# Kernel tuning notes

Hardware: AMD Instinct MI355X
Metric: run time of the kernel (lower is better)

The kernel has to match this reference:

```python
import jax, jax.numpy as jnp
import numpy as np

D = 1024
K = 3  # depthwise conv kernel size, causal (left pad K-1)


def setup_inputs() -> dict:
    key = jax.random.key(0)
    ks = jax.random.split(key, 6)
    B, L = 16, 2048
    x = jax.random.normal(ks[0], (B, L, D), dtype=jnp.float32)
    s_in = 1.0 / np.sqrt(D)
    Win = jax.random.uniform(ks[1], (3 * D, D), minval=-s_in, maxval=s_in, dtype=jnp.float32)
    bin_ = jax.random.uniform(ks[2], (3 * D,), minval=-s_in, maxval=s_in, dtype=jnp.float32)
    # depthwise Conv1d weight (D, 1, K) -> stored as (D, K)
    s_c = 1.0 / np.sqrt(K)  # fan_in = in_channels/groups * K = K
    wconv = jax.random.uniform(ks[3], (D, K), minval=-s_c, maxval=s_c, dtype=jnp.float32)
    Wout = jax.random.uniform(ks[4], (D, D), minval=-s_in, maxval=s_in, dtype=jnp.float32)
    bout = jax.random.uniform(ks[5], (D,), minval=-s_in, maxval=s_in, dtype=jnp.float32)
    return {"x": x, "Win": Win, "bin_": bin_, "wconv": wconv, "Wout": Wout, "bout": bout}


def reference(x, Win, bin_, wconv, Wout, bout):
    # x: (B, L, D). in_proj -> (B, L, 3D); chunk along channel dim == last dim here
    BCx = jnp.einsum('bld,ed->ble', x, Win) + bin_
    Bg, Cg, xg = jnp.split(BCx, 3, axis=-1)  # each (B, L, D)
    Bx = Bg * xg
    L = Bx.shape[1]
    # causal depthwise conv: pad K-1 zeros on the left of time axis
    xp = jnp.pad(Bx, ((0, 0), (K - 1, 0), (0, 0)))
    conv_out = (wconv[:, 0] * xp[:, 0:L]
                + wconv[:, 1] * xp[:, 1:L + 1]
                + wconv[:, 2] * xp[:, 2:L + 2])  # (B, L, D)
    y = Cg * conv_out
    return jnp.einsum('bld,ed->ble', y, Wout) + bout
```

## Files before the change

kernel.cpp:

```cpp
#include <hip/hip_runtime.h>
#include <hip/hip_bf16.h>

#define D_    1024
#define LSEQ  2048
#define M_    32768
#define K_    1024
#define NT    16

typedef __bf16 bf16x8 __attribute__((ext_vector_type(8)));
typedef float  f32x4  __attribute__((ext_vector_type(4)));

__device__ __forceinline__ unsigned short f2bf(float f) {
  unsigned u = __float_as_uint(f);
  u += 0x7FFFu + ((u >> 16) & 1u);
  return (unsigned short)(u >> 16);
}
__device__ __forceinline__ float bf2f(unsigned short h) {
  return __uint_as_float(((unsigned)h) << 16);
}

__device__ __forceinline__ void gload_lds16(const void* g, void* l) {
  __builtin_amdgcn_global_load_lds((const __attribute__((address_space(1))) void*)g,
                                   (__attribute__((address_space(3))) void*)l,
                                   16, 0, 0);
}

#define FENCE() asm volatile("" ::: "memory")
#define RBAR()  do { FENCE(); __builtin_amdgcn_s_barrier(); FENCE(); } while (0)

#define NX4  (M_ * K_ / 4)
#define NW4  (3072 * K_ / 4)
#define NO4  (D_ * K_ / 4)
__global__ __launch_bounds__(256) void cvt_all(const float* __restrict__ x,
                                               const float* __restrict__ Win,
                                               const float* __restrict__ Wout,
                                               unsigned short* __restrict__ x_b,
                                               unsigned short* __restrict__ Win_b,
                                               unsigned short* __restrict__ Wout_b) {
  int i = blockIdx.x * 256 + threadIdx.x;
  const float* src;
  unsigned short* dst;
  int off;
  if (i < NX4)            { src = x;    dst = x_b;    off = i; }
  else if (i < NX4 + NW4) { src = Win;  dst = Win_b;  off = i - NX4; }
  else                    { src = Wout; dst = Wout_b; off = i - NX4 - NW4; }
  float4 v = ((const float4*)src)[off];
  ushort4 o;
  o.x = f2bf(v.x); o.y = f2bf(v.y); o.z = f2bf(v.z); o.w = f2bf(v.w);
  ((ushort4*)dst)[off] = o;
}


__device__ __forceinline__ void gemm_core256(char* smem,
    const unsigned short* aBase,
    const unsigned short* b0p, const unsigned short* b1p,
    const unsigned short* b2p, const unsigned short* b3p,
    f32x4 acc[8][4]) {
  const int tid  = threadIdx.x;
  const int lane = tid & 63;
  const int wm   = (tid >> 6) >> 2;
  const int wn   = (tid >> 6) & 3;
  const int quad = lane >> 4;
  const int l16  = lane & 15;
  const int swz  = (quad ^ (l16 & 7)) << 4;
  const int aRow = ((wm << 7) + l16) * 128 + swz;
  const int bRow = ((wn << 6) + l16) * 128 + swz;

  auto STAGE = [&](int t) {
    char* lb = smem + ((t & 1) << 16);
    const int k0 = t << 6;
#pragma unroll
    for (int i = 0; i < 4; ++i)
      gload_lds16(aBase + ((long)i << 16) + k0, lb + tid * 16 + i * 8192);
    gload_lds16(b0p + k0, lb + 32768 + tid * 16);
    gload_lds16(b1p + k0, lb + 32768 + tid * 16 + 8192);
    gload_lds16(b2p + k0, lb + 32768 + tid * 16 + 16384);
    gload_lds16(b3p + k0, lb + 32768 + tid * 16 + 24576);
  };

  STAGE(0);
  STAGE(1);
  asm volatile("s_waitcnt vmcnt(8)" ::: "memory");
  RBAR();

  bf16x8 av[4][2], b0[2][2], b1[2][2];

  for (int t = 0; t < NT; ++t) {
    const char* As = smem + ((t & 1) << 16);
    const char* Bs = As + 32768;

#pragma unroll
    for (int f = 0; f < 2; ++f) {
      const int o = bRow + f * 2048;
      b0[f][0] = *(const bf16x8*)(Bs + o);
      b0[f][1] = *(const bf16x8*)(Bs + (o ^ 64));
    }
#pragma unroll
    for (int f = 0; f < 4; ++f) {
      const int o = aRow + f * 2048;
      av[f][0] = *(const bf16x8*)(As + o);
      av[f][1] = *(const bf16x8*)(As + (o ^ 64));
    }
#pragma unroll
    for (int f = 0; f < 2; ++f) {
      const int o = bRow + (2 + f) * 2048;
      b1[f][0] = *(const bf16x8*)(Bs + o);
      b1[f][1] = *(const bf16x8*)(Bs + (o ^ 64));
    }
    RBAR();

    __builtin_amdgcn_s_setprio(1);
#pragma unroll
    for (int f = 0; f < 4; ++f)
#pragma unroll
      for (int gg = 0; gg < 2; ++gg) {
        f32x4 c = acc[f][gg];
        c = __builtin_amdgcn_mfma_f32_16x16x32_bf16(av[f][0], b0[gg][0], c, 0, 0, 0);
        c = __builtin_amdgcn_mfma_f32_16x16x32_bf16(av[f][1], b0[gg][1], c, 0, 0, 0);
        acc[f][gg] = c;
      }
    __builtin_amdgcn_s_setprio(0);
    RBAR();

    __builtin_amdgcn_s_setprio(1);
#pragma unroll
    for (int f = 0; f < 4; ++f) {
#pragma unroll
      for (int gg = 0; gg < 2; ++gg) {
        f32x4 c = acc[f][2 + gg];
        c = __builtin_amdgcn_mfma_f32_16x16x32_bf16(av[f][0], b1[gg][0], c, 0, 0, 0);
        c = __builtin_amdgcn_mfma_f32_16x16x32_bf16(av[f][1], b1[gg][1], c, 0, 0, 0);
        acc[f][2 + gg] = c;
      }
      const int o = aRow + (4 + f) * 2048;
      av[f][0] = *(const bf16x8*)(As + o);
      av[f][1] = *(const bf16x8*)(As + (o ^ 64));
    }
    __builtin_amdgcn_s_setprio(0);
    RBAR();

    __builtin_amdgcn_s_setprio(1);
#pragma unroll
    for (int f = 0; f < 4; ++f)
#pragma unroll
      for (int gg = 0; gg < 2; ++gg) {
        f32x4 c = acc[4 + f][2 + gg];
        c = __builtin_amdgcn_mfma_f32_16x16x32_bf16(av[f][0], b1[gg][0], c, 0, 0, 0);
        c = __builtin_amdgcn_mfma_f32_16x16x32_bf16(av[f][1], b1[gg][1], c, 0, 0, 0);
        acc[4 + f][2 + gg] = c;
      }
    __builtin_amdgcn_s_setprio(0);
    RBAR();

    if (t + 2 < NT) STAGE(t + 2);
    __builtin_amdgcn_s_setprio(1);
#pragma unroll
    for (int f = 0; f < 4; ++f)
#pragma unroll
      for (int gg = 0; gg < 2; ++gg) {
        f32x4 c = acc[4 + f][gg];
        c = __builtin_amdgcn_mfma_f32_16x16x32_bf16(av[f][0], b0[gg][0], c, 0, 0, 0);
        c = __builtin_amdgcn_mfma_f32_16x16x32_bf16(av[f][1], b0[gg][1], c, 0, 0, 0);
        acc[4 + f][gg] = c;
      }
    __builtin_amdgcn_s_setprio(0);

    if (t + 2 < NT) {
      asm volatile("s_waitcnt vmcnt(8)" ::: "memory");
      RBAR();
    } else if (t + 2 == NT) {
      asm volatile("s_waitcnt vmcnt(0)" ::: "memory");
      RBAR();
    }
  }
}

__global__ __launch_bounds__(512, 2) void gemm_inproj(const unsigned short* __restrict__ A,
                                                      const unsigned short* __restrict__ Wb,
                                                      const float* __restrict__ bin,
                                                      unsigned short* __restrict__ Bx,
                                                      unsigned short* __restrict__ Cg) {
  __shared__ __align__(16) char smem[131072];

  const int g  = blockIdx.x;
  const int u  = g >> 3;
  const int m0 = ((g & 7) + 8 * (u / 12)) * 256;
  const int c  = u % 12;
  const bool paired = (c < 8);

  const int tid  = threadIdx.x;
  const int lane = tid & 63;
  const int srow = ((tid >> 6) << 3) + (lane >> 3);
  const int sch  = (lane & 7) ^ (lane >> 3);

  const unsigned short* aBase = A + (long)(m0 + srow) * K_ + sch * 8;
  const unsigned short *b0p, *b1p, *b2p, *b3p;
  int n0;
  if (paired) {
    n0  = c * 128;
    b0p = Wb + (long)(n0 + srow) * K_ + sch * 8;
    b1p = b0p + (long)64 * K_;
    b2p = Wb + (long)(2048 + n0 + srow) * K_ + sch * 8;
    b3p = b2p + (long)64 * K_;
  } else {
    n0  = (c - 8) * 256;
    b0p = Wb + (long)(1024 + n0 + srow) * K_ + sch * 8;
    b1p = b0p + (long)64 * K_;
    b2p = b0p + (long)128 * K_;
    b3p = b0p + (long)192 * K_;
  }

  f32x4 acc[8][4] = {};
  gemm_core256(smem, aBase, b0p, b1p, b2p, b3p, acc);

  const int wm = (tid >> 6) >> 2, wn = (tid >> 6) & 3;
  const int quad = lane >> 4, l16 = lane & 15;
  float* tr = (float*)smem;

  float bvv[4];
#pragma unroll
  for (int ni = 0; ni < 4; ++ni) {
    int col = wn * 64 + ni * 16 + l16;
    bvv[ni] = paired ? ((col < 128) ? bin[n0 + col] : bin[2048 + n0 + col - 128])
                     : bin[1024 + n0 + col];
  }

  const int trr   = tid >> 4;
  const int tcc   = tid & 15;
  const int growb = m0 + ((trr >> 4) << 7) + (trr & 15);

#pragma unroll
  for (int mi = 0; mi < 8; ++mi) {
    __syncthreads();
#pragma unroll
    for (int ni = 0; ni < 4; ++ni) {
      int col = wn * 64 + ni * 16 + l16;
      f32x4 v = acc[mi][ni];
#pragma unroll
      for (int r = 0; r < 4; ++r)
        tr[(wm * 16 + quad * 4 + r) * 260 + col] = v[r] + bvv[ni];
    }
    __syncthreads();

    const int grow = growb + mi * 16;
    if (paired) {
#pragma unroll
      for (int j = 0; j < 2; ++j) {
        int cc = tcc * 4 + j * 64;
        f32x4 bg = *(const f32x4*)&tr[trr * 260 + cc];
        f32x4 xg = *(const f32x4*)&tr[trr * 260 + 128 + cc];
        ushort4 o;
        o.x = f2bf(bg[0] * xg[0]); o.y = f2bf(bg[1] * xg[1]);
        o.z = f2bf(bg[2] * xg[2]); o.w = f2bf(bg[3] * xg[3]);
        *(ushort4*)&Bx[(long)grow * D_ + n0 + cc] = o;
      }
    } else {
#pragma unroll
      for (int j = 0; j < 4; ++j) {
        int cc = tcc * 4 + j * 64;
        f32x4 v = *(const f32x4*)&tr[trr * 260 + cc];
        ushort4 o;
        o.x = f2bf(v[0]); o.y = f2bf(v[1]); o.z = f2bf(v[2]); o.w = f2bf(v[3]);
        *(ushort4*)&Cg[(long)grow * D_ + n0 + cc] = o;
      }
    }
  }
}

__global__ __launch_bounds__(256) void conv_mul(const unsigned short* __restrict__ Bx,
                                                const unsigned short* __restrict__ Cg,
                                                const float* __restrict__ wconv,
                                                unsigned short* __restrict__ y) {
  __shared__ float wt[3][D_];
  for (int i = threadIdx.x; i < D_; i += 256) {
    wt[0][i] = wconv[i * 3 + 0];
    wt[1][i] = wconv[i * 3 + 1];
    wt[2][i] = wconv[i * 3 + 2];
  }
  __syncthreads();

  int idx = blockIdx.x * 256 + threadIdx.x;
  int bl  = idx >> 7;
  int d8  = (idx & 127) * 8;
  int l   = bl & (LSEQ - 1);

  typedef unsigned short us8 __attribute__((ext_vector_type(8)));
  us8 zz = {0, 0, 0, 0, 0, 0, 0, 0};
  us8 x0 = *(const us8*)&Bx[(long)bl * D_ + d8];
  us8 x1 = (l >= 1) ? *(const us8*)&Bx[(long)(bl - 1) * D_ + d8] : zz;
  us8 x2 = (l >= 2) ? *(const us8*)&Bx[(long)(bl - 2) * D_ + d8] : zz;
  us8 cg = *(const us8*)&Cg[(long)bl * D_ + d8];

  us8 o;
#pragma unroll
  for (int j = 0; j < 8; ++j) {
    float conv = wt[0][d8 + j] * bf2f(x2[j]) + wt[1][d8 + j] * bf2f(x1[j])
               + wt[2][d8 + j] * bf2f(x0[j]);
    o[j] = f2bf(bf2f(cg[j]) * conv);
  }
  *(us8*)&y[(long)bl * D_ + d8] = o;
}

__global__ __launch_bounds__(512, 2) void gemm_out(const unsigned short* __restrict__ A,
                                                   const unsigned short* __restrict__ Wb,
                                                   const float* __restrict__ bias,
                                                   float* __restrict__ Out) {
  __shared__ __align__(16) char smem[131072];

  const int g  = blockIdx.x;
  const int u  = g >> 3;
  const int m0 = ((g & 7) + 8 * (u >> 2)) * 256;
  const int n0 = (u & 3) * 256;

  const int tid  = threadIdx.x;
  const int lane = tid & 63;
  const int srow = ((tid >> 6) << 3) + (lane >> 3);
  const int sch  = (lane & 7) ^ (lane >> 3);

  const unsigned short* aBase = A + (long)(m0 + srow) * K_ + sch * 8;
  const unsigned short* b0p   = Wb + (long)(n0 + srow) * K_ + sch * 8;

  f32x4 acc[8][4] = {};
  gemm_core256(smem, aBase, b0p, b0p + (long)64 * K_, b0p + (long)128 * K_,
               b0p + (long)192 * K_, acc);

  const int wm = (tid >> 6) >> 2, wn = (tid >> 6) & 3;
  const int quad = lane >> 4, l16 = lane & 15;
  float* tr = (float*)smem;

  float bvv[4];
#pragma unroll
  for (int ni = 0; ni < 4; ++ni)
    bvv[ni] = bias[n0 + wn * 64 + ni * 16 + l16];

  const int trr   = tid >> 4;
  const int tcc   = tid & 15;
  const int growb = m0 + ((trr >> 4) << 7) + (trr & 15);

#pragma unroll
  for (int mi = 0; mi < 8; ++mi) {
    __syncthreads();
#pragma unroll
    for (int ni = 0; ni < 4; ++ni) {
      int col = wn * 64 + ni * 16 + l16;
      f32x4 v = acc[mi][ni];
#pragma unroll
      for (int r = 0; r < 4; ++r)
        tr[(wm * 16 + quad * 4 + r) * 260 + col] = v[r] + bvv[ni];
    }
    __syncthreads();

    const int grow = growb + mi * 16;
#pragma unroll
    for (int j = 0; j < 4; ++j) {
      int cc = tcc * 4 + j * 64;
      *(f32x4*)&Out[(long)grow * D_ + n0 + cc] = *(const f32x4*)&tr[trr * 260 + cc];
    }
  }
}

extern "C" void kernel_launch(void* const* d_in, const int* in_sizes, int n_in,
                              void* d_out, int out_size, void* d_ws, size_t ws_size,
                              hipStream_t stream) {
  const float* x     = (const float*)d_in[0];
  const float* Win   = (const float*)d_in[1];
  const float* bin   = (const float*)d_in[2];
  const float* wconv = (const float*)d_in[3];
  const float* Wout  = (const float*)d_in[4];
  const float* bout  = (const float*)d_in[5];

  char* ws = (char*)d_ws;
  unsigned short* x_b    = (unsigned short*)(ws);
  unsigned short* Win_b  = (unsigned short*)(ws + 67108864);
  unsigned short* Wout_b = (unsigned short*)(ws + 73400320);
  unsigned short* Bx_b   = (unsigned short*)(ws + 75497472);
  unsigned short* Cg_b   = (unsigned short*)(ws + 142606336);
  unsigned short* y_b    = (unsigned short*)(ws + 209715200);

  cvt_all<<<(NX4 + NW4 + NO4) / 256, 256, 0, stream>>>(x, Win, Wout, x_b, Win_b, Wout_b);

  gemm_inproj<<<1536, 512, 0, stream>>>(x_b, Win_b, bin, Bx_b, Cg_b);

  conv_mul<<<(M_ * (D_ / 8)) / 256, 256, 0, stream>>>(Bx_b, Cg_b, wconv, y_b);

  gemm_out<<<512, 512, 0, stream>>>(y_b, Wout_b, bout, (float*)d_out);
}
```

Baseline: 546.6 us.

## Restructure GEMM k-loop to cut per-iteration barriers and interleave LDS reads

Rewrites the main k-loop of the bf16 MFMA GEMM. Per-iteration block barriers drop from about five to two, and the second half of the A fragments goes into separate registers (av1) so reads and MFMAs interleave without barriers between quadrants. The prefetch wait now happens before the last MFMA quadrant instead of after it, so the global-load wait is more exposed. In exchange the kernel holds more live vector registers, which under launch_bounds(512,2) risks spills or lower occupancy.

```diff
diff --git a/kernel.cpp b/kernel.cpp
--- a/kernel.cpp
+++ b/kernel.cpp
@@ -83,11 +83,11 @@
   asm volatile("s_waitcnt vmcnt(8)" ::: "memory");
   RBAR();
 
-  bf16x8 av[4][2], b0[2][2], b1[2][2];
-
   for (int t = 0; t < NT; ++t) {
     const char* As = smem + ((t & 1) << 16);
     const char* Bs = As + 32768;
+
+    bf16x8 b0[2][2], b1[2][2], av0[4][2], av1[4][2];
 
 #pragma unroll
     for (int f = 0; f < 2; ++f) {
@@ -98,80 +98,81 @@
 #pragma unroll
     for (int f = 0; f < 4; ++f) {
       const int o = aRow + f * 2048;
-      av[f][0] = *(const bf16x8*)(As + o);
-      av[f][1] = *(const bf16x8*)(As + (o ^ 64));
-    }
+      av0[f][0] = *(const bf16x8*)(As + o);
+      av0[f][1] = *(const bf16x8*)(As + (o ^ 64));
+    }
+
+    __builtin_amdgcn_s_setprio(1);
+#pragma unroll
+    for (int f = 0; f < 4; ++f)
+#pragma unroll
+      for (int gg = 0; gg < 2; ++gg) {
+        f32x4 c = acc[f][gg];
+        c = __builtin_amdgcn_mfma_f32_16x16x32_bf16(av0[f][0], b0[gg][0], c, 0, 0, 0);
+        c = __builtin_amdgcn_mfma_f32_16x16x32_bf16(av0[f][1], b0[gg][1], c, 0, 0, 0);
+        acc[f][gg] = c;
+      }
+    __builtin_amdgcn_s_setprio(0);
+
 #pragma unroll
     for (int f = 0; f < 2; ++f) {
       const int o = bRow + (2 + f) * 2048;
       b1[f][0] = *(const bf16x8*)(Bs + o);
       b1[f][1] = *(const bf16x8*)(Bs + (o ^ 64));
     }
-    RBAR();
-
     __builtin_amdgcn_s_setprio(1);
 #pragma unroll
     for (int f = 0; f < 4; ++f)
-#pragma unroll
-      for (int gg = 0; gg < 2; ++gg) {
-        f32x4 c = acc[f][gg];
-        c = __builtin_amdgcn_mfma_f32_16x16x32_bf16(av[f][0], b0[gg][0], c, 0, 0, 0);
-        c = __builtin_amdgcn_mfma_f32_16x16x32_bf16(av[f][1], b0[gg][1], c, 0, 0, 0);
-        acc[f][gg] = c;
-      }
-    __builtin_amdgcn_s_setprio(0);
-    RBAR();
-
-    __builtin_amdgcn_s_setprio(1);
-#pragma unroll
-    for (int f = 0; f < 4; ++f) {
 #pragma unroll
       for (int gg = 0; gg < 2; ++gg) {
         f32x4 c = acc[f][2 + gg];
-        c = __builtin_amdgcn_mfma_f32_16x16x32_bf16(av[f][0], b1[gg][0], c, 0, 0, 0);
-        c = __builtin_amdgcn_mfma_f32_16x16x32_bf16(av[f][1], b1[gg][1], c, 0, 0, 0);
+        c = __builtin_amdgcn_mfma_f32_16x16x32_bf16(av0[f][0], b1[gg][0], c, 0, 0, 0);
+        c = __builtin_amdgcn_mfma_f32_16x16x32_bf16(av0[f][1], b1[gg][1], c, 0, 0, 0);
         acc[f][2 + gg] = c;
       }
+    __builtin_amdgcn_s_setprio(0);
+
+#pragma unroll
+    for (int f = 0; f < 4; ++f) {
       const int o = aRow + (4 + f) * 2048;
-      av[f][0] = *(const bf16x8*)(As + o);
-      av[f][1] = *(const bf16x8*)(As + (o ^ 64));
-    }
-    __builtin_amdgcn_s_setprio(0);
-    RBAR();
-
+      av1[f][0] = *(const bf16x8*)(As + o);
+      av1[f][1] = *(const bf16x8*)(As + (o ^ 64));
+    }
     __builtin_amdgcn_s_setprio(1);
 #pragma unroll
     for (int f = 0; f < 4; ++f)
 #pragma unroll
       for (int gg = 0; gg < 2; ++gg) {
         f32x4 c = acc[4 + f][2 + gg];
-        c = __builtin_amdgcn_mfma_f32_16x16x32_bf16(av[f][0], b1[gg][0], c, 0, 0, 0);
-        c = __builtin_amdgcn_mfma_f32_16x16x32_bf16(av[f][1], b1[gg][1], c, 0, 0, 0);
+        c = __builtin_amdgcn_mfma_f32_16x16x32_bf16(av1[f][0], b1[gg][0], c, 0, 0, 0);
+        c = __builtin_amdgcn_mfma_f32_16x16x32_bf16(av1[f][1], b1[gg][1], c, 0, 0, 0);
         acc[4 + f][2 + gg] = c;
       }
     __builtin_amdgcn_s_setprio(0);
+
+    asm volatile("s_waitcnt lgkmcnt(0)" ::: "memory");
+    __builtin_amdgcn_sched_barrier(0);
     RBAR();
 
-    if (t + 2 < NT) STAGE(t + 2);
+    if (t + 2 < NT) {
+      STAGE(t + 2);
+      asm volatile("s_waitcnt vmcnt(8)" ::: "memory");
+    } else {
+      asm volatile("s_waitcnt vmcnt(0)" ::: "memory");
+    }
+    RBAR();
+
     __builtin_amdgcn_s_setprio(1);
 #pragma unroll
     for (int f = 0; f < 4; ++f)
 #pragma unroll
       for (int gg = 0; gg < 2; ++gg) {
         f32x4 c = acc[4 + f][gg];
-        c = __builtin_amdgcn_mfma_f32_16x16x32_bf16(av[f][0], b0[gg][0], c, 0, 0, 0);
-        c = __builtin_amdgcn_mfma_f32_16x16x32_bf16(av[f][1], b0[gg][1], c, 0, 0, 0);
+        c = __builtin_amdgcn_mfma_f32_16x16x32_bf16(av1[f][0], b0[gg][0], c, 0, 0, 0);
+        c = __builtin_amdgcn_mfma_f32_16x16x32_bf16(av1[f][1], b0[gg][1], c, 0, 0, 0);
         acc[4 + f][gg] = c;
       }
     __builtin_amdgcn_s_setprio(0);
-
-    if (t + 2 < NT) {
-      asm volatile("s_waitcnt vmcnt(8)" ::: "memory");
-      RBAR();
-    } else if (t + 2 == NT) {
-      asm volatile("s_waitcnt vmcnt(0)" ::: "memory");
-      RBAR();
-    }
   }
 }
 
```

New measurement: 537.6 us. Within noise of the previous version (-1.6%).
